# Kernel tuning notes

Hardware: AMD Instinct MI355X
Metric: run time of the kernel (lower is better)

## Reference

```python
import jax, jax.numpy as jnp
import numpy as np

B, S0 = 16, 511
D = 512    # encoder_output_dim
HG = 256   # graph_rnn_hidden_graph
HE = 256   # graph_rnn_hidden_edge (must equal HG: h_prev[0] = graph_state)
T = 128    # tag_representation_dim
M = 32     # graph_rnn_m
S = S0 + 1 # after head-sentinel prepend


def setup_inputs() -> dict:
    ks = iter(jax.random.split(jax.random.key(0), 40))
    def U(shape, fan):
        # torch RNN/Linear default init: U(-1/sqrt(fan), 1/sqrt(fan))
        return jax.random.uniform(next(ks), shape, jnp.float32, -1.0, 1.0) / np.sqrt(fan)
    return {
        'input': jax.random.normal(next(ks), (B, S0, D), jnp.float32),
        'sentinel': jax.random.normal(next(ks), (D,), jnp.float32),
        'g_Wih0': U((HG, D), HG), 'g_Whh0': U((HG, HG), HG), 'g_bih0': U((HG,), HG), 'g_bhh0': U((HG,), HG),
        'g_Wih1': U((HG, HG), HG), 'g_Whh1': U((HG, HG), HG), 'g_bih1': U((HG,), HG), 'g_bhh1': U((HG,), HG),
        'e_Wih0': U((HE, 1), HE), 'e_Whh0': U((HE, HE), HE), 'e_bih0': U((HE,), HE), 'e_bhh0': U((HE,), HE),
        'e_Wih1': U((HE, HE), HE), 'e_Whh1': U((HE, HE), HE), 'e_bih1': U((HE,), HE), 'e_bhh1': U((HE,), HE),
        'cls_W': U((1, HE), HE), 'cls_b': U((1,), HE),
        'head_W': U((T, HG), HG), 'head_b': U((T,), HG),
        'dep_W': U((T, HG), HG), 'dep_b': U((T,), HG),
        'mask': jnp.ones((B, S0), jnp.int32),
        'head_indices': jax.random.randint(next(ks), (B, S0), 0, S0, jnp.int32),
    }


def _rnn_layer(x, W_ih, W_hh, b_ih, b_hh):
    # Elman RNN layer (tanh), batch_first, h0 = 0. x: [B, S, Din] -> [B, S, H]
    xw = jnp.einsum('bsd,hd->bsh', x, W_ih) + b_ih + b_hh  # hoist input GEMM out of scan
    h0 = jnp.zeros((x.shape[0], W_hh.shape[0]), x.dtype)
    def step(h, xw_t):
        h = jnp.tanh(xw_t + h @ W_hh.T)
        return h, h
    _, ys = jax.lax.scan(step, h0, jnp.swapaxes(xw, 0, 1))
    return jnp.swapaxes(ys, 0, 1)


def _forward(input, sentinel, g_Wih0, g_Whh0, g_bih0, g_bhh0, g_Wih1, g_Whh1, g_bih1, g_bhh1,
             e_Wih0, e_Whh0, e_bih0, e_bhh0, e_Wih1, e_Whh1, e_bih1, e_bhh1,
             cls_W, cls_b, head_W, head_b, dep_W, dep_b, mask, head_indices):
    Bv = input.shape[0]
    # prepend head sentinel / prepend_ones
    x = jnp.concatenate([jnp.broadcast_to(sentinel, (Bv, 1, D)), input], axis=1)   # [B,S,D]
    mask_f = jnp.concatenate([jnp.ones((Bv, 1), mask.dtype), mask], axis=1)        # [B,S]
    # graph_pass: 2-layer tanh RNN; pad_packed_sequence zeroes padded timesteps
    h = _rnn_layer(x, g_Wih0, g_Whh0, g_bih0, g_bhh0)
    gs = _rnn_layer(h, g_Wih1, g_Whh1, g_bih1, g_bhh1)                             # [B,S,HG]
    gs = gs * mask_f[..., None].astype(gs.dtype)
    N = Bv * S
    gt = gs.reshape(N, HG)
    def estep(carry, _):
        xe, h0, h1 = carry
        h0 = jnp.tanh(xe @ e_Wih0.T + e_bih0 + e_bhh0 + h0 @ e_Whh0.T)
        h1 = jnp.tanh(h0 @ e_Wih1.T + e_bih1 + e_bhh1 + h1 @ e_Whh1.T)
        p = jax.nn.sigmoid(h1 @ cls_W.T + cls_b)   # [N,1]
        return (p, h0, h1), p[:, 0]
    init = (jnp.ones((N, 1), gs.dtype), gt, jnp.zeros((N, HE), gs.dtype))
    _, probs = jax.lax.scan(estep, init, None, length=M)                           # [M,N]
    A = jnp.concatenate([jnp.ones((1, N), gs.dtype), probs], axis=0).T.reshape(Bv, S, M + 1)
    # reshape_adj: scatter the M-band back into a [B,S,S] matrix, then transpose
    Ab = A[:, :, 1:]                                                               # [B,S,M]
    i = jnp.arange(S)[:, None]
    j = jnp.arange(S)[None, :]
    start = jnp.maximum(0, i - M)
    valid = (j >= start) & (j < i)
    midx = jnp.clip(j - start, 0, M - 1)                                           # [S,S]
    gathered = Ab[:, jnp.arange(S)[:, None], midx]                                 # [B,S,S]
    arc_logits = jnp.swapaxes(jnp.where(valid[None], gathered, jnp.zeros((), gs.dtype)), 1, 2)
    # tag heads (dropout = identity at inference)
    head_tag = jax.nn.elu(jnp.einsum('bsh,th->bst', gs, head_W) + head_b)
    dep_tag = jax.nn.elu(jnp.einsum('bsh,th->bst', gs, dep_W) + dep_b)
    return head_tag, dep_tag, arc_logits


def reference(input, sentinel, g_Wih0, g_Whh0, g_bih0, g_bhh0, g_Wih1, g_Whh1, g_bih1, g_bhh1,
              e_Wih0, e_Whh0, e_bih0, e_bhh0, e_Wih1, e_Whh1, e_bih1, e_bhh1,
              cls_W, cls_b, head_W, head_b, dep_W, dep_b, mask, head_indices):
    return _forward(input, sentinel, g_Wih0, g_Whh0, g_bih0, g_bhh0, g_Wih1, g_Whh1, g_bih1, g_bhh1,
                    e_Wih0, e_Whh0, e_bih0, e_bhh0, e_Wih1, e_Whh1, e_bih1, e_bhh1,
                    cls_W, cls_b, head_W, head_b, dep_W, dep_b, mask, head_indices)
```

## Files before the change

kernel.cpp:

```cpp
#include <hip/hip_runtime.h>

typedef unsigned short u16;
typedef short s8v __attribute__((ext_vector_type(8)));
typedef float f4v __attribute__((ext_vector_type(4)));

__device__ __forceinline__ float bf2f(u16 s) {
  unsigned u = ((unsigned)s) << 16;
  return __builtin_bit_cast(float, u);
}
__device__ __forceinline__ u16 f2bf(float f) {
  unsigned u = __builtin_bit_cast(unsigned, f);
  unsigned r = u + 0x7fffu + ((u >> 16) & 1u);
  return (u16)(r >> 16);
}
__device__ __forceinline__ s8v load8bf(const u16* p) {
  return __builtin_bit_cast(s8v, *(const uint4*)p);
}
__device__ __forceinline__ f4v mfma16(s8v a, s8v b, f4v c) {
  return __builtin_amdgcn_mfma_f32_16x16x32_bf16(a, b, c, 0, 0, 0);
}
__device__ __forceinline__ s8v pin8(s8v x) {
  union { s8v v; unsigned u[4]; } t;
  t.v = x;
  asm volatile("" : "+v"(t.u[0]), "+v"(t.u[1]), "+v"(t.u[2]), "+v"(t.u[3]));
  return t.v;
}
__device__ __forceinline__ void barrier_lds() {
  asm volatile("s_waitcnt lgkmcnt(0)\n\ts_barrier" ::: "memory");
}
__device__ __forceinline__ void cvt8(const float* p, s8v& hi, s8v& lo) {
  float4 x0 = ((const float4*)p)[0];
  float4 x1 = ((const float4*)p)[1];
  float v[8] = {x0.x, x0.y, x0.z, x0.w, x1.x, x1.y, x1.z, x1.w};
  union { s8v v; u16 a[8]; } H, L;
#pragma unroll
  for (int i = 0; i < 8; ++i) {
    u16 h = f2bf(v[i]);
    H.a[i] = h;
    L.a[i] = f2bf(v[i] - bf2f(h));
  }
  hi = H.v;
  lo = L.v;
}
__device__ __forceinline__ float fast_tanh(float x) {
  float t = __builtin_amdgcn_exp2f(x * 2.885390081777927f);
  return 1.f - 2.f * __builtin_amdgcn_rcpf(t + 1.f);
}
__device__ __forceinline__ float fast_sigmoid(float x) {
  float t = __builtin_amdgcn_exp2f(x * -1.4426950408889634f);
  return __builtin_amdgcn_rcpf(1.f + t);
}

__global__ void k_prep(const float* __restrict__ W0, const float* __restrict__ W1,
                       u16* __restrict__ whh0b, u16* __restrict__ whh1b,
                       const float* __restrict__ E0, const float* __restrict__ E1,
                       const float* __restrict__ E2, u16* __restrict__ B0,
                       u16* __restrict__ B1, u16* __restrict__ B2,
                       const float* __restrict__ gW0, u16* __restrict__ gw0hi,
                       u16* __restrict__ gw0lo, const float* __restrict__ gW1,
                       u16* __restrict__ gw1hi, u16* __restrict__ gw1lo,
                       const float* __restrict__ hW, u16* __restrict__ hWhi,
                       u16* __restrict__ hWlo, const float* __restrict__ dW,
                       u16* __restrict__ dWhi, u16* __restrict__ dWlo,
                       const int* __restrict__ mask, float* __restrict__ maskfb) {
  int t = blockIdx.x * 256 + threadIdx.x;
  if (t < 131072) {
    int layer = t >> 16;
    int idx = t & 65535;
    const float* W = layer ? W1 : W0;
    u16* dst = layer ? whh1b : whh0b;
    dst[idx] = f2bf(W[idx]);
  } else if (t < 327680) {
    int c = t - 131072;
    int which = c >> 16;
    int idx = c & 65535;
    const float* src = which == 0 ? E0 : (which == 1 ? E1 : E2);
    u16* dst = which == 0 ? B0 : (which == 1 ? B1 : B2);
    dst[idx] = f2bf(src[idx]);
  } else if (t < 589824) {
    const float* src;
    u16 *dhi, *dlo;
    int idx;
    if (t < 458752) { idx = t - 327680; src = gW0; dhi = gw0hi; dlo = gw0lo; }
    else if (t < 524288) { idx = t - 458752; src = gW1; dhi = gw1hi; dlo = gw1lo; }
    else if (t < 557056) { idx = t - 524288; src = hW; dhi = hWhi; dlo = hWlo; }
    else { idx = t - 557056; src = dW; dhi = dWhi; dlo = dWlo; }
    float v = src[idx];
    u16 h = f2bf(v);
    dhi[idx] = h;
    dlo[idx] = f2bf(v - bf2f(h));
  } else if (t < 598016) {
    int c = t - 589824;
    int s = c >> 4, b = c & 15;
    maskfb[c] = (s == 0) ? 1.f : (float)mask[b * 511 + s - 1];
  }
}

__launch_bounds__(256)
__global__ void k_xw0(const float* __restrict__ input, const float* __restrict__ sentinel,
                      const u16* __restrict__ Whi, const u16* __restrict__ Wlo,
                      const float* __restrict__ b1, const float* __restrict__ b2,
                      float* __restrict__ outxw) {
  const int l = threadIdx.x & 63;
  const int wv = threadIdx.x >> 6;
  const int l15 = l & 15, q = l >> 4;
  const int row0 = blockIdx.x * 64 + wv * 16;
  const int col0 = blockIdx.y * 64;
  int row = row0 + l15;
  int s = row & 511, b = row >> 9;
  const float* aptr = (s == 0) ? sentinel : input + (((size_t)(b * 511 + s - 1)) << 9);
  f4v acc[4];
#pragma unroll
  for (int i = 0; i < 4; ++i) acc[i] = (f4v){0.f, 0.f, 0.f, 0.f};
#pragma unroll
  for (int kt = 0; kt < 16; ++kt) {
    int k0 = kt * 32 + q * 8;
    s8v ah, al;
    cvt8(aptr + k0, ah, al);
#pragma unroll
    for (int nt = 0; nt < 4; ++nt) {
      int j = col0 + nt * 16 + l15;
      s8v wh = load8bf(Whi + ((size_t)j << 9) + k0);
      s8v wl = load8bf(Wlo + ((size_t)j << 9) + k0);
      acc[nt] = mfma16(ah, wh, acc[nt]);
      acc[nt] = mfma16(al, wh, acc[nt]);
      acc[nt] = mfma16(ah, wl, acc[nt]);
    }
  }
#pragma unroll
  for (int nt = 0; nt < 4; ++nt) {
    int col = col0 + nt * 16 + l15;
    float bias = b1[col] + b2[col];
#pragma unroll
    for (int r = 0; r < 4; ++r) {
      int rr = row0 + q * 4 + r;
      outxw[((size_t)rr << 8) + col] = acc[nt][r] + bias;
    }
  }
}

__launch_bounds__(256)
__global__ void k_gemm(const float* __restrict__ A, const u16* __restrict__ Whi,
                       const u16* __restrict__ Wlo, const float* __restrict__ b1,
                       const float* __restrict__ b2, float* __restrict__ outf,
                       int K, int J, int act) {
  const int l = threadIdx.x & 63;
  const int wv = threadIdx.x >> 6;
  const int l15 = l & 15, q = l >> 4;
  const int row0 = blockIdx.x * 64 + wv * 16;
  const int col0 = blockIdx.y * 64;
  const float* aptr = A + (size_t)(row0 + l15) * K;
  f4v acc[4];
#pragma unroll
  for (int i = 0; i < 4; ++i) acc[i] = (f4v){0.f, 0.f, 0.f, 0.f};
  const int nkt = K >> 5;
  for (int kt = 0; kt < nkt; ++kt) {
    int k0 = kt * 32 + q * 8;
    s8v ah, al;
    cvt8(aptr + k0, ah, al);
#pragma unroll
    for (int nt = 0; nt < 4; ++nt) {
      int j = col0 + nt * 16 + l15;
      s8v wh = load8bf(Whi + (size_t)j * K + k0);
      s8v wl = load8bf(Wlo + (size_t)j * K + k0);
      acc[nt] = mfma16(ah, wh, acc[nt]);
      acc[nt] = mfma16(al, wh, acc[nt]);
      acc[nt] = mfma16(ah, wl, acc[nt]);
    }
  }
#pragma unroll
  for (int nt = 0; nt < 4; ++nt) {
    int col = col0 + nt * 16 + l15;
    float bias = b1[col] + (b2 ? b2[col] : 0.f);
#pragma unroll
    for (int r = 0; r < 4; ++r) {
      int rr = row0 + q * 4 + r;
      float v = acc[nt][r] + bias;
      if (act) v = v > 0.f ? v : (__builtin_amdgcn_exp2f(v * 1.4426950408889634f) - 1.f);
      outf[(size_t)rr * J + col] = v;
    }
  }
}

__launch_bounds__(512, 2)
__global__ void k_scan_f(const float* __restrict__ xw, const u16* __restrict__ W0b,
                         const u16* __restrict__ Wxb, const u16* __restrict__ W1b,
                         const float* __restrict__ bih1, const float* __restrict__ bhh1,
                         float* __restrict__ outf, const float* __restrict__ maskf) {
  __shared__ u16 H1[2][272];
  __shared__ u16 H2[2][272];
  __shared__ float XW2[2][272];
  __shared__ float mtab[512];
  const int tid = threadIdx.x;
  const int l = tid & 63, wv = tid >> 6;
  const int l15 = l & 15, q = l >> 4;
  const int b = blockIdx.x;

  s8v w0[2][8], wx[2][8], w1[2][8];
#pragma unroll
  for (int nt = 0; nt < 2; ++nt) {
    int j = wv * 32 + nt * 16 + l15;
#pragma unroll
    for (int kt = 0; kt < 8; ++kt) {
      int off = (j << 8) + kt * 32 + q * 8;
      w0[nt][kt] = pin8(load8bf(W0b + off));
      wx[nt][kt] = pin8(load8bf(Wxb + off));
      w1[nt][kt] = pin8(load8bf(W1b + off));
    }
  }
  if (tid < 256) {
    H1[0][tid] = 0; H1[1][tid] = 0;
    H2[0][tid] = 0; H2[1][tid] = 0;
    XW2[0][tid] = 0.f; XW2[1][tid] = 0.f;
  }
  if (tid < 512) mtab[tid] = maskf[tid * 16 + b];

  const int j0 = wv * 32 + l15;
  float b2v[2];
#pragma unroll
  for (int nt = 0; nt < 2; ++nt) b2v[nt] = bih1[j0 + nt * 16] + bhh1[j0 + nt * 16];
  __syncthreads();

  const size_t nbase = (size_t)b << 9;
  const float* xrow = xw + (nbase << 8);
  const int q0 = (q == 0);

  float xA[2], xB[2];
#pragma unroll
  for (int nt = 0; nt < 2; ++nt) {
    xA[nt] = xrow[j0 + nt * 16];
    xB[nt] = xrow[256 + j0 + nt * 16];
  }

  auto STEP = [&](int g, int par, float* xc) {
    const u16* H1r = &H1[par][0];
    const u16* H2r = &H2[par][0];
    f4v a1[2], ax[2], a2[2];
#pragma unroll
    for (int nt = 0; nt < 2; ++nt) {
      a1[nt] = (f4v){xc[nt], 0.f, 0.f, 0.f};
      ax[nt] = (f4v){b2v[nt], 0.f, 0.f, 0.f};
      a2[nt] = (f4v){XW2[par][j0 + nt * 16], 0.f, 0.f, 0.f};
    }
#pragma unroll
    for (int kt = 0; kt < 8; ++kt) {
      s8v h1b = load8bf(H1r + kt * 32 + q * 8);
#pragma unroll
      for (int nt = 0; nt < 2; ++nt) {
        a1[nt] = mfma16(h1b, w0[nt][kt], a1[nt]);
        ax[nt] = mfma16(h1b, wx[nt][kt], ax[nt]);
      }
    }
#pragma unroll
    for (int kt = 0; kt < 8; ++kt) {
      s8v h2b = load8bf(H2r + kt * 32 + q * 8);
#pragma unroll
      for (int nt = 0; nt < 2; ++nt) a2[nt] = mfma16(h2b, w1[nt][kt], a2[nt]);
    }
    if (g < 512) {
      u16* Hw = &H1[1 - par][0];
#pragma unroll
      for (int nt = 0; nt < 2; ++nt) {
        float h = fast_tanh(a1[nt][0]);
        if (q0) Hw[j0 + nt * 16] = f2bf(h);
      }
    }
    if (g >= 1 && g < 513) {
      float* Xw = &XW2[1 - par][0];
#pragma unroll
      for (int nt = 0; nt < 2; ++nt)
        if (q0) Xw[j0 + nt * 16] = ax[nt][0];
    }
    if (g >= 2) {
      int t = g - 2;
      float mf = mtab[t];
      u16* Hw = &H2[1 - par][0];
      float* orow = outf + ((nbase + t) << 8);
#pragma unroll
      for (int nt = 0; nt < 2; ++nt) {
        float h = fast_tanh(a2[nt][0]);
        if (q0) {
          Hw[j0 + nt * 16] = f2bf(h);
          orow[j0 + nt * 16] = h * mf;
        }
      }
    }
  };

  for (int g = 0; g < 514; g += 2) {
    STEP(g, 0, xA);
    int sp = g + 2; if (sp > 511) sp = 511;
#pragma unroll
    for (int nt = 0; nt < 2; ++nt) xA[nt] = xrow[(sp << 8) + j0 + nt * 16];
    barrier_lds();
    STEP(g + 1, 1, xB);
    int sq = g + 3; if (sq > 511) sq = 511;
#pragma unroll
    for (int nt = 0; nt < 2; ++nt) xB[nt] = xrow[(sq << 8) + j0 + nt * 16];
    barrier_lds();
  }
}

__launch_bounds__(512, 2)
__global__ void k_enc(const float* __restrict__ gs,
                      const u16* __restrict__ W0b, const u16* __restrict__ W1b,
                      const u16* __restrict__ W2b, const float* __restrict__ wih0,
                      const float* __restrict__ bih0, const float* __restrict__ bhh0,
                      const float* __restrict__ bih1, const float* __restrict__ bhh1,
                      const float* __restrict__ clsW, const float* __restrict__ clsb,
                      float* __restrict__ Ab) {
  __shared__ __align__(16) u16 hA0[32 * 264];
  __shared__ __align__(16) u16 hA1[32 * 264];
  __shared__ float xe[32];
  __shared__ float b0v[256], w0v[256], b1v[256], clsv[256];
  __shared__ float clsbs;
  const int tid = threadIdx.x;
  const int n0 = blockIdx.x * 32;

  for (int c = tid; c < 8192; c += 512) {
    int row = c >> 8, col = c & 255;
    hA0[row * 264 + col] = f2bf(gs[(((size_t)(n0 + row)) << 8) + col]);
    hA1[row * 264 + col] = 0;
  }
  if (tid < 256) {
    b0v[tid] = bih0[tid] + bhh0[tid];
    w0v[tid] = wih0[tid];
    b1v[tid] = bih1[tid] + bhh1[tid];
    clsv[tid] = clsW[tid];
  }
  if (tid < 32) xe[tid] = 1.0f;
  if (tid == 0) clsbs = clsb[0];

  const int l = tid & 63, wv = tid >> 6;
  const int l15 = l & 15, q = l >> 4;
  const int colbase = wv * 32;

  s8v w0[2][8], w1[2][8], w2[2][8];
#pragma unroll
  for (int nt = 0; nt < 2; ++nt) {
    int jj = colbase + nt * 16 + l15;
#pragma unroll
    for (int kt = 0; kt < 8; ++kt) {
      int off = (jj << 8) + kt * 32 + q * 8;
      w0[nt][kt] = load8bf(W0b + off);
      w1[nt][kt] = load8bf(W1b + off);
      w2[nt][kt] = load8bf(W2b + off);
    }
  }
  __syncthreads();

  for (int m = 0; m < 32; ++m) {
    f4v acc[2][2];
#pragma unroll
    for (int mt = 0; mt < 2; ++mt)
#pragma unroll
      for (int nt = 0; nt < 2; ++nt) acc[mt][nt] = (f4v){0.f, 0.f, 0.f, 0.f};
#pragma unroll
    for (int kt = 0; kt < 8; ++kt) {
#pragma unroll
      for (int mt = 0; mt < 2; ++mt) {
        s8v a = __builtin_bit_cast(s8v, *(const uint4*)&hA0[(mt * 16 + l15) * 264 + kt * 32 + q * 8]);
        acc[mt][0] = mfma16(a, w0[0][kt], acc[mt][0]);
        acc[mt][1] = mfma16(a, w0[1][kt], acc[mt][1]);
      }
    }
    __syncthreads();
#pragma unroll
    for (int nt = 0; nt < 2; ++nt) {
      int col = colbase + nt * 16 + l15;
      float wc = w0v[col], bc = b0v[col];
#pragma unroll
      for (int mt = 0; mt < 2; ++mt)
#pragma unroll
        for (int r = 0; r < 4; ++r) {
          int row = mt * 16 + q * 4 + r;
          float v = acc[mt][nt][r] + xe[row] * wc + bc;
          hA0[row * 264 + col] = f2bf(fast_tanh(v));
        }
    }
    __syncthreads();
#pragma unroll
    for (int mt = 0; mt < 2; ++mt)
#pragma unroll
      for (int nt = 0; nt < 2; ++nt) acc[mt][nt] = (f4v){0.f, 0.f, 0.f, 0.f};
#pragma unroll
    for (int kt = 0; kt < 8; ++kt) {
#pragma unroll
      for (int mt = 0; mt < 2; ++mt) {
        s8v a0 = __builtin_bit_cast(s8v, *(const uint4*)&hA0[(mt * 16 + l15) * 264 + kt * 32 + q * 8]);
        s8v a1 = __builtin_bit_cast(s8v, *(const uint4*)&hA1[(mt * 16 + l15) * 264 + kt * 32 + q * 8]);
        acc[mt][0] = mfma16(a0, w1[0][kt], acc[mt][0]);
        acc[mt][1] = mfma16(a0, w1[1][kt], acc[mt][1]);
        acc[mt][0] = mfma16(a1, w2[0][kt], acc[mt][0]);
        acc[mt][1] = mfma16(a1, w2[1][kt], acc[mt][1]);
      }
    }
    __syncthreads();
#pragma unroll
    for (int nt = 0; nt < 2; ++nt) {
      int col = colbase + nt * 16 + l15;
      float bc = b1v[col];
#pragma unroll
      for (int mt = 0; mt < 2; ++mt)
#pragma unroll
        for (int r = 0; r < 4; ++r) {
          int row = mt * 16 + q * 4 + r;
          float v = acc[mt][nt][r] + bc;
          hA1[row * 264 + col] = f2bf(fast_tanh(v));
        }
    }
    __syncthreads();
    if (tid < 256) {
      int row = tid >> 3, seg = tid & 7;
      float sum = 0.f;
#pragma unroll
      for (int u = 0; u < 4; ++u) {
        int col = seg * 32 + u * 8;
#pragma unroll
        for (int e = 0; e < 8; ++e) sum += bf2f(hA1[row * 264 + col + e]) * clsv[col + e];
      }
      sum += __shfl_down(sum, 4, 8);
      sum += __shfl_down(sum, 2, 8);
      sum += __shfl_down(sum, 1, 8);
      if (seg == 0) {
        float pp = fast_sigmoid(sum + clsbs);
        xe[row] = pp;
        Ab[(((size_t)(n0 + row)) << 5) + m] = pp;
      }
    }
    __syncthreads();
  }
}

__global__ void k_arc(const float* __restrict__ Ab, float* __restrict__ out2) {
  int t = blockIdx.x * 256 + threadIdx.x;
  int b = t >> 18;
  int rem = t & 262143;
  int j = rem >> 9, i = rem & 511;
  int start = i - 32;
  if (start < 0) start = 0;
  float v = 0.f;
  if (j >= start && j < i) v = Ab[((((size_t)b << 9) + i) << 5) + (j - start)];
  out2[t] = v;
}

extern "C" void kernel_launch(void* const* d_in, const int* in_sizes, int n_in,
                              void* d_out, int out_size, void* d_ws, size_t ws_size,
                              hipStream_t stream) {
  const float* input    = (const float*)d_in[0];
  const float* sentinel = (const float*)d_in[1];
  const float* g_Wih0   = (const float*)d_in[2];
  const float* g_Whh0   = (const float*)d_in[3];
  const float* g_bih0   = (const float*)d_in[4];
  const float* g_bhh0   = (const float*)d_in[5];
  const float* g_Wih1   = (const float*)d_in[6];
  const float* g_Whh1   = (const float*)d_in[7];
  const float* g_bih1   = (const float*)d_in[8];
  const float* g_bhh1   = (const float*)d_in[9];
  const float* e_Wih0   = (const float*)d_in[10];
  const float* e_Whh0   = (const float*)d_in[11];
  const float* e_bih0   = (const float*)d_in[12];
  const float* e_bhh0   = (const float*)d_in[13];
  const float* e_Wih1   = (const float*)d_in[14];
  const float* e_Whh1   = (const float*)d_in[15];
  const float* e_bih1   = (const float*)d_in[16];
  const float* e_bhh1   = (const float*)d_in[17];
  const float* cls_W    = (const float*)d_in[18];
  const float* cls_b    = (const float*)d_in[19];
  const float* head_W   = (const float*)d_in[20];
  const float* head_b   = (const float*)d_in[21];
  const float* dep_W    = (const float*)d_in[22];
  const float* dep_b    = (const float*)d_in[23];
  const int* mask       = (const int*)d_in[24];

  float* out = (float*)d_out;
  char* ws = (char*)d_ws;
  float* xw_buf = (float*)ws;
  float* gsb    = (float*)(ws + (16u << 20));
  float* Ab     = (float*)(ws + (24u << 20));
  size_t o = (25u << 20);
  u16* whh0b   = (u16*)(ws + o); o += 128u << 10;
  u16* whh1b   = (u16*)(ws + o); o += 128u << 10;
  float* maskfb= (float*)(ws + o); o += 32u << 10;
  u16* eb0     = (u16*)(ws + o); o += 128u << 10;
  u16* eb1     = (u16*)(ws + o); o += 128u << 10;
  u16* eb2     = (u16*)(ws + o); o += 128u << 10;
  u16* gw0hi   = (u16*)(ws + o); o += 256u << 10;
  u16* gw0lo   = (u16*)(ws + o); o += 256u << 10;
  u16* gw1hi   = (u16*)(ws + o); o += 128u << 10;
  u16* gw1lo   = (u16*)(ws + o); o += 128u << 10;
  u16* hWhi    = (u16*)(ws + o); o += 64u << 10;
  u16* hWlo    = (u16*)(ws + o); o += 64u << 10;
  u16* dWhi    = (u16*)(ws + o); o += 64u << 10;
  u16* dWlo    = (u16*)(ws + o); o += 64u << 10;

  k_prep<<<2336, 256, 0, stream>>>(g_Whh0, g_Whh1, whh0b, whh1b, e_Whh0, e_Wih1, e_Whh1,
                                   eb0, eb1, eb2, g_Wih0, gw0hi, gw0lo, g_Wih1, gw1hi,
                                   gw1lo, head_W, hWhi, hWlo, dep_W, dWhi, dWlo,
                                   mask, maskfb);
  k_xw0<<<dim3(128, 4), 256, 0, stream>>>(input, sentinel, gw0hi, gw0lo, g_bih0, g_bhh0,
                                          xw_buf);
  k_scan_f<<<16, 512, 0, stream>>>(xw_buf, whh0b, gw1hi, whh1b, g_bih1, g_bhh1,
                                   gsb, maskfb);
  k_gemm<<<dim3(128, 2), 256, 0, stream>>>(gsb, hWhi, hWlo, head_b, nullptr, out,
                                           256, 128, 1);
  k_gemm<<<dim3(128, 2), 256, 0, stream>>>(gsb, dWhi, dWlo, dep_b, nullptr, out + 1048576,
                                           256, 128, 1);
  k_enc<<<256, 512, 0, stream>>>(gsb, eb0, eb1, eb2, e_Wih0, e_bih0, e_bhh0,
                                 e_bih1, e_bhh1, cls_W, cls_b, Ab);
  k_arc<<<16384, 256, 0, stream>>>(Ab, out + 2097152);
}
```

Before: 852.3 us.

## Specialize scan waves by role and merge head/dep GEMM launches

The scan kernel's per-wave work split changes. Before, every wave computed 2 column tiles of each of the three matrix products (layer-0 recurrence, layer-1 input projection, layer-1 recurrence). Now each wave handles 6 column tiles assigned by role through a templated body, so some waves do only layer-0 recurrence and others only layer-1 work. The aim is to shorten the critical layer-0 chain per step and cut redundant LDS reads of H1 and H2, at the cost of uneven load across waves and more register pressure. Separately, the two tag-head GEMM launches become one launch that uses blockIdx.z to pick the weights, removing one launch.

```diff
diff --git a/kernel.cpp b/kernel.cpp
--- a/kernel.cpp
+++ b/kernel.cpp
@@ -140,10 +140,16 @@
 }
 
 __launch_bounds__(256)
-__global__ void k_gemm(const float* __restrict__ A, const u16* __restrict__ Whi,
-                       const u16* __restrict__ Wlo, const float* __restrict__ b1,
-                       const float* __restrict__ b2, float* __restrict__ outf,
-                       int K, int J, int act) {
+__global__ void k_gemm2(const float* __restrict__ A,
+                        const u16* __restrict__ WhiA, const u16* __restrict__ WloA,
+                        const float* __restrict__ bA, float* __restrict__ outA,
+                        const u16* __restrict__ WhiB, const u16* __restrict__ WloB,
+                        const float* __restrict__ bB, float* __restrict__ outB,
+                        int K, int J) {
+  const u16* Whi = blockIdx.z ? WhiB : WhiA;
+  const u16* Wlo = blockIdx.z ? WloB : WloA;
+  const float* b1 = blockIdx.z ? bB : bA;
+  float* outf = blockIdx.z ? outB : outA;
   const int l = threadIdx.x & 63;
   const int wv = threadIdx.x >> 6;
   const int l15 = l & 15, q = l >> 4;
@@ -171,14 +177,132 @@
 #pragma unroll
   for (int nt = 0; nt < 4; ++nt) {
     int col = col0 + nt * 16 + l15;
-    float bias = b1[col] + (b2 ? b2[col] : 0.f);
+    float bias = b1[col];
 #pragma unroll
     for (int r = 0; r < 4; ++r) {
       int rr = row0 + q * 4 + r;
       float v = acc[nt][r] + bias;
-      if (act) v = v > 0.f ? v : (__builtin_amdgcn_exp2f(v * 1.4426950408889634f) - 1.f);
+      v = v > 0.f ? v : (__builtin_amdgcn_exp2f(v * 1.4426950408889634f) - 1.f);
       outf[(size_t)rr * J + col] = v;
     }
+  }
+}
+
+template <int NR1, int NX2, int NR2>
+__device__ __forceinline__ void scan_body(
+    int tid0, int l15, int q, const float* __restrict__ xrow,
+    const u16* __restrict__ W0b, const u16* __restrict__ Wxb,
+    const u16* __restrict__ W1b, const float* __restrict__ bih1,
+    const float* __restrict__ bhh1, float* __restrict__ outf,
+    u16 (*H1)[272], u16 (*H2)[272], float (*XW2)[272], float* mtab,
+    size_t nbase) {
+  constexpr int NH1 = NR1 + NX2;
+  const int q0 = (q == 0);
+
+  int col[6];
+#pragma unroll
+  for (int d = 0; d < 6; ++d) col[d] = (((tid0 + d) & 15) << 4) + l15;
+
+  s8v w[6][8];
+#pragma unroll
+  for (int d = 0; d < 6; ++d) {
+    const u16* wb = (d < NR1) ? W0b : ((d < NH1) ? Wxb : W1b);
+#pragma unroll
+    for (int kt = 0; kt < 8; ++kt)
+      w[d][kt] = pin8(load8bf(wb + (col[d] << 8) + kt * 32 + q * 8));
+  }
+
+  float b2v[6];
+#pragma unroll
+  for (int d = NR1; d < NH1; ++d) b2v[d] = bih1[col[d]] + bhh1[col[d]];
+
+  float xA[6], xB[6];
+#pragma unroll
+  for (int d = 0; d < NR1; ++d) {
+    xA[d] = xrow[col[d]];
+    xB[d] = xrow[256 + col[d]];
+  }
+
+  __syncthreads();
+
+  f4v acc[6];
+#pragma unroll
+  for (int d = 0; d < 6; ++d) acc[d] = (f4v){0.f, 0.f, 0.f, 0.f};
+
+  auto STEP = [&](int g, int par, float* xc) {
+#pragma unroll
+    for (int d = 0; d < NR1; ++d) acc[d][0] = xc[d];
+#pragma unroll
+    for (int d = NR1; d < NH1; ++d) acc[d][0] = b2v[d];
+#pragma unroll
+    for (int d = NH1; d < 6; ++d) acc[d][0] = XW2[par][col[d]];
+
+    if constexpr (NH1 > 0) {
+      const u16* H1r = &H1[par][0];
+#pragma unroll
+      for (int kt = 0; kt < 8; ++kt) {
+        s8v hb = load8bf(H1r + kt * 32 + q * 8);
+#pragma unroll
+        for (int d = 0; d < NH1; ++d) acc[d] = mfma16(hb, w[d][kt], acc[d]);
+      }
+    }
+    if constexpr (NR2 > 0) {
+      const u16* H2r = &H2[par][0];
+#pragma unroll
+      for (int kt = 0; kt < 8; ++kt) {
+        s8v hb = load8bf(H2r + kt * 32 + q * 8);
+#pragma unroll
+        for (int d = NH1; d < 6; ++d) acc[d] = mfma16(hb, w[d][kt], acc[d]);
+      }
+    }
+
+    if (q0) {
+      if constexpr (NR1 > 0) {
+        if (g < 512) {
+          u16* Hw = &H1[1 - par][0];
+#pragma unroll
+          for (int d = 0; d < NR1; ++d) Hw[col[d]] = f2bf(fast_tanh(acc[d][0]));
+        }
+      }
+      if constexpr (NX2 > 0) {
+        if (g >= 1 && g < 513) {
+          float* Xw = &XW2[1 - par][0];
+#pragma unroll
+          for (int d = NR1; d < NH1; ++d) Xw[col[d]] = acc[d][0];
+        }
+      }
+      if constexpr (NR2 > 0) {
+        if (g >= 2) {
+          int t = g - 2;
+          float mf = mtab[t];
+          u16* Hw = &H2[1 - par][0];
+          float* orow = outf + ((nbase + t) << 8);
+#pragma unroll
+          for (int d = NH1; d < 6; ++d) {
+            float h = fast_tanh(acc[d][0]);
+            Hw[col[d]] = f2bf(h);
+            orow[col[d]] = h * mf;
+          }
+        }
+      }
+    }
+  };
+
+  for (int g = 0; g < 514; g += 2) {
+    STEP(g, 0, xA);
+    if constexpr (NR1 > 0) {
+      int sp = g + 2; if (sp > 511) sp = 511;
+#pragma unroll
+      for (int d = 0; d < NR1; ++d) xA[d] = xrow[(sp << 8) + col[d]];
+    }
+    barrier_lds();
+    STEP(g + 1, 1, xB);
+    if constexpr (NR1 > 0) {
+      int sq = g + 3; if (sq > 511) sq = 511;
+#pragma unroll
+      for (int d = 0; d < NR1; ++d) xB[d] = xrow[(sq << 8) + col[d]];
+    }
+    barrier_lds();
   }
 }
 
@@ -196,18 +320,6 @@
   const int l15 = l & 15, q = l >> 4;
   const int b = blockIdx.x;
 
-  s8v w0[2][8], wx[2][8], w1[2][8];
-#pragma unroll
-  for (int nt = 0; nt < 2; ++nt) {
-    int j = wv * 32 + nt * 16 + l15;
-#pragma unroll
-    for (int kt = 0; kt < 8; ++kt) {
-      int off = (j << 8) + kt * 32 + q * 8;
-      w0[nt][kt] = pin8(load8bf(W0b + off));
-      wx[nt][kt] = pin8(load8bf(Wxb + off));
-      w1[nt][kt] = pin8(load8bf(W1b + off));
-    }
-  }
   if (tid < 256) {
     H1[0][tid] = 0; H1[1][tid] = 0;
     H2[0][tid] = 0; H2[1][tid] = 0;
@@ -215,89 +327,33 @@
   }
   if (tid < 512) mtab[tid] = maskf[tid * 16 + b];
 
-  const int j0 = wv * 32 + l15;
-  float b2v[2];
-#pragma unroll
-  for (int nt = 0; nt < 2; ++nt) b2v[nt] = bih1[j0 + nt * 16] + bhh1[j0 + nt * 16];
-  __syncthreads();
-
   const size_t nbase = (size_t)b << 9;
   const float* xrow = xw + (nbase << 8);
-  const int q0 = (q == 0);
-
-  float xA[2], xB[2];
-#pragma unroll
-  for (int nt = 0; nt < 2; ++nt) {
-    xA[nt] = xrow[j0 + nt * 16];
-    xB[nt] = xrow[256 + j0 + nt * 16];
-  }
-
-  auto STEP = [&](int g, int par, float* xc) {
-    const u16* H1r = &H1[par][0];
-    const u16* H2r = &H2[par][0];
-    f4v a1[2], ax[2], a2[2];
-#pragma unroll
-    for (int nt = 0; nt < 2; ++nt) {
-      a1[nt] = (f4v){xc[nt], 0.f, 0.f, 0.f};
-      ax[nt] = (f4v){b2v[nt], 0.f, 0.f, 0.f};
-      a2[nt] = (f4v){XW2[par][j0 + nt * 16], 0.f, 0.f, 0.f};
-    }
-#pragma unroll
-    for (int kt = 0; kt < 8; ++kt) {
-      s8v h1b = load8bf(H1r + kt * 32 + q * 8);
-#pragma unroll
-      for (int nt = 0; nt < 2; ++nt) {
-        a1[nt] = mfma16(h1b, w0[nt][kt], a1[nt]);
-        ax[nt] = mfma16(h1b, wx[nt][kt], ax[nt]);
-      }
-    }
-#pragma unroll
-    for (int kt = 0; kt < 8; ++kt) {
-      s8v h2b = load8bf(H2r + kt * 32 + q * 8);
-#pragma unroll
-      for (int nt = 0; nt < 2; ++nt) a2[nt] = mfma16(h2b, w1[nt][kt], a2[nt]);
-    }
-    if (g < 512) {
-      u16* Hw = &H1[1 - par][0];
-#pragma unroll
-      for (int nt = 0; nt < 2; ++nt) {
-        float h = fast_tanh(a1[nt][0]);
-        if (q0) Hw[j0 + nt * 16] = f2bf(h);
-      }
-    }
-    if (g >= 1 && g < 513) {
-      float* Xw = &XW2[1 - par][0];
-#pragma unroll
-      for (int nt = 0; nt < 2; ++nt)
-        if (q0) Xw[j0 + nt * 16] = ax[nt][0];
-    }
-    if (g >= 2) {
-      int t = g - 2;
-      float mf = mtab[t];
-      u16* Hw = &H2[1 - par][0];
-      float* orow = outf + ((nbase + t) << 8);
-#pragma unroll
-      for (int nt = 0; nt < 2; ++nt) {
-        float h = fast_tanh(a2[nt][0]);
-        if (q0) {
-          Hw[j0 + nt * 16] = f2bf(h);
-          orow[j0 + nt * 16] = h * mf;
-        }
-      }
-    }
-  };
-
-  for (int g = 0; g < 514; g += 2) {
-    STEP(g, 0, xA);
-    int sp = g + 2; if (sp > 511) sp = 511;
-#pragma unroll
-    for (int nt = 0; nt < 2; ++nt) xA[nt] = xrow[(sp << 8) + j0 + nt * 16];
-    barrier_lds();
-    STEP(g + 1, 1, xB);
-    int sq = g + 3; if (sq > 511) sq = 511;
-#pragma unroll
-    for (int nt = 0; nt < 2; ++nt) xB[nt] = xrow[(sq << 8) + j0 + nt * 16];
-    barrier_lds();
+  const int tid0 = wv * 6;
+
+  switch (wv) {
+    case 0:
+    case 1:
+      scan_body<6, 0, 0>(tid0, l15, q, xrow, W0b, Wxb, W1b, bih1, bhh1, outf,
+                         H1, H2, XW2, mtab, nbase);
+      break;
+    case 2:
+      scan_body<4, 2, 0>(tid0, l15, q, xrow, W0b, Wxb, W1b, bih1, bhh1, outf,
+                         H1, H2, XW2, mtab, nbase);
+      break;
+    case 3:
+    case 4:
+      scan_body<0, 6, 0>(tid0, l15, q, xrow, W0b, Wxb, W1b, bih1, bhh1, outf,
+                         H1, H2, XW2, mtab, nbase);
+      break;
+    case 5:
+      scan_body<0, 2, 4>(tid0, l15, q, xrow, W0b, Wxb, W1b, bih1, bhh1, outf,
+                         H1, H2, XW2, mtab, nbase);
+      break;
+    default:
+      scan_body<0, 0, 6>(tid0, l15, q, xrow, W0b, Wxb, W1b, bih1, bhh1, outf,
+                         H1, H2, XW2, mtab, nbase);
+      break;
   }
 }
 
@@ -502,10 +558,9 @@
                                           xw_buf);
   k_scan_f<<<16, 512, 0, stream>>>(xw_buf, whh0b, gw1hi, whh1b, g_bih1, g_bhh1,
                                    gsb, maskfb);
-  k_gemm<<<dim3(128, 2), 256, 0, stream>>>(gsb, hWhi, hWlo, head_b, nullptr, out,
-                                           256, 128, 1);
-  k_gemm<<<dim3(128, 2), 256, 0, stream>>>(gsb, dWhi, dWlo, dep_b, nullptr, out + 1048576,
-                                           256, 128, 1);
+  k_gemm2<<<dim3(128, 2, 2), 256, 0, stream>>>(gsb, hWhi, hWlo, head_b, out,
+                                               dWhi, dWlo, dep_b, out + 1048576,
+                                               256, 128);
   k_enc<<<256, 512, 0, stream>>>(gsb, eb0, eb1, eb2, e_Wih0, e_bih0, e_bhh0,
                                  e_bih1, e_bhh1, cls_W, cls_b, Ab);
   k_arc<<<16384, 256, 0, stream>>>(Ab, out + 2097152);
```

New measurement: 1.061 ms. 1.25x slower.
